# Optimization experiments

Measured on AMD Instinct MI355X. Metric: run time of the kernel, lower is better.

## Reference

```python
import jax, jax.numpy as jnp
import numpy as np
import math

B, L, E, H, G = 2, 128, 1024, 16, 8
D = E // H   # head_dim = 64
R = H // G   # query heads per kv head = 2


def setup_inputs() -> dict:
    key = jax.random.key(0)
    ks = jax.random.split(key, 12)
    def nrm(k, shape, s=1.0):
        return jax.random.normal(k, shape, dtype=jnp.float32) * s
    return {
        "Q": nrm(ks[0], (B, L, E)),
        "K": nrm(ks[1], (B, L, E)),
        "V": nrm(ks[2], (B, L, E)),
        "rpe": nrm(ks[3], (B, L, L, E)),
        "ln_g": jnp.ones((E,), jnp.float32),
        "ln_b": jnp.zeros((E,), jnp.float32),
        "Wq": nrm(ks[4], (E, H * D), 0.02), "bq": jnp.zeros((H * D,), jnp.float32),
        "Wk": nrm(ks[5], (E, G * D), 0.02), "bk": jnp.zeros((G * D,), jnp.float32),
        "Wv": nrm(ks[6], (E, G * D), 0.02), "bv": jnp.zeros((G * D,), jnp.float32),
        "Wrk": nrm(ks[7], (E, G * D), 0.02), "brk": jnp.zeros((G * D,), jnp.float32),
        "Wrv": nrm(ks[8], (E, G * D), 0.02), "brv": jnp.zeros((G * D,), jnp.float32),
        "Wo": nrm(ks[9], (E, E), 0.02), "bo": jnp.zeros((E,), jnp.float32),
    }


def _layernorm(x, g, b, eps=1e-5):
    mu = jnp.mean(x, axis=-1, keepdims=True)
    var = jnp.var(x, axis=-1, keepdims=True)
    return (x - mu) * jax.lax.rsqrt(var + eps) * g + b


def reference(Q, K, V, rpe, ln_g, ln_b, Wq, bq, Wk, bk, Wv, bv, Wrk, brk, Wrv, brv, Wo, bo):
    q = (Q @ Wq + bq).reshape(B, L, H, D).transpose(0, 2, 1, 3)   # [B,H,L,D]
    k = (K @ Wk + bk).reshape(B, L, G, D).transpose(0, 2, 1, 3)   # [B,G,L,D]
    v = (V @ Wv + bv).reshape(B, L, G, D).transpose(0, 2, 1, 3)   # [B,G,L,D]

    rn = _layernorm(rpe, ln_g, ln_b)                              # [B,L,L,E]
    rpe_k = (rn @ Wrk + brk).reshape(B, L, L, G, D).transpose(0, 3, 1, 2, 4)  # [B,G,L,L,D]
    rpe_v = (rn @ Wrv + brv).reshape(B, L, L, G, D).transpose(0, 3, 1, 2, 4)

    # Group query heads: head h = g*R + r maps to kv group g (repeat_interleave semantics).
    qg = q.reshape(B, G, R, L, D)
    # score[b,h,i,j] = q[b,h,i] . (k[b,g,i] + rpe_k[b,g,i,j]) / sqrt(D)
    # (note: the original pairs q_i with k_i, only rpe_k carries j-dependence)
    base = jnp.einsum('bgrid,bgid->bgri', qg, k)                  # j-independent q.k
    cross = jnp.einsum('bgrid,bgijd->bgrij', qg, rpe_k)
    scores = (base[..., None] + cross) / math.sqrt(D)             # [B,G,R,L,L]

    # Faithful to F.softmax over flattened L*L axis per head.
    attn = jax.nn.softmax(scores.reshape(B, G, R, L * L), axis=-1).reshape(B, G, R, L, L)

    # qv[b,h,i] = sum_j attn[b,h,i,j] * (v[b,g,i] + rpe_v[b,g,i,j])
    wsum = jnp.sum(attn, axis=-1)                                 # [B,G,R,L]
    qv = wsum[..., None] * v[:, :, None] + jnp.einsum('bgrij,bgijd->bgrid', attn, rpe_v)
    qv = qv.reshape(B, H, L, D).transpose(0, 2, 1, 3).reshape(B, L, E)
    return qv @ Wo + bo
```

## Files before the change

### kernel.cpp

```cpp
#include <hip/hip_runtime.h>


__global__ __launch_bounds__(256) void k_zero(
    const float* __restrict__ bq, const float* __restrict__ bk, const float* __restrict__ bv,
    const float* __restrict__ bo,
    float* __restrict__ q_ws, float* __restrict__ k_ws, float* __restrict__ v_ws,
    float* __restrict__ qv_ws, float* __restrict__ out, float* __restrict__ Gu_ws)
{
  int rr = blockIdx.x, tid = threadIdx.x;
#pragma unroll
  for (int s = 0; s < 4; s++) {
    int i = tid + s * 256;
    q_ws[rr * 1024 + i] = bq[i];
    qv_ws[rr * 1024 + i] = 0.f;
    out[rr * 1024 + i] = bo[i];
  }
#pragma unroll
  for (int s = 0; s < 2; s++) {
    int i = tid + s * 256;
    k_ws[rr * 512 + i] = bk[i];
    v_ws[rr * 512 + i] = bv[i];
  }
  int t = rr * 256 + tid;
  if (t < 4096) Gu_ws[t] = 0.f;
}

__global__ __launch_bounds__(256) void k_qkv(
    const float* __restrict__ Q, const float* __restrict__ K, const float* __restrict__ V,
    const float* __restrict__ Wq, const float* __restrict__ Wk, const float* __restrict__ Wv,
    float* __restrict__ q_ws, float* __restrict__ k_ws, float* __restrict__ v_ws)
{
  __shared__ float xs[8][256];
  int ct = blockIdx.x, rt = blockIdx.y, es = blockIdx.z, tid = threadIdx.x;
  const float* X; const float* W; float* out; int ldW, ldO, c0;
  if (ct < 4)      { X = Q; W = Wq; out = q_ws; ldW = 1024; ldO = 1024; c0 = ct * 256; }
  else if (ct < 6) { X = K; W = Wk; out = k_ws; ldW = 512;  ldO = 512;  c0 = (ct - 4) * 256; }
  else             { X = V; W = Wv; out = v_ws; ldW = 512;  ldO = 512;  c0 = (ct - 6) * 256; }
  int row0 = rt * 8, e0 = es * 256;
  for (int f = tid; f < 512; f += 256) {
    int r = f >> 6, e4 = f & 63;
    *(float4*)&xs[r][e4 * 4] = *(const float4*)(X + (size_t)(row0 + r) * 1024 + e0 + e4 * 4);
  }
  __syncthreads();
  int cg = tid & 63, rs = tid >> 6;
  int c = c0 + cg * 4;
  const float* wp = W + (size_t)e0 * ldW + c;
  float a0[4] = {0, 0, 0, 0}, a1[4] = {0, 0, 0, 0};
  float4 wc = *(const float4*)wp;
  for (int e = 0; e < 256; e++) {
    int en = e + 1 < 256 ? e + 1 : 255;
    float4 wn = *(const float4*)(wp + (size_t)en * ldW);
    float x0 = xs[rs][e], x1 = xs[rs + 4][e];
    a0[0] += x0 * wc.x; a0[1] += x0 * wc.y; a0[2] += x0 * wc.z; a0[3] += x0 * wc.w;
    a1[0] += x1 * wc.x; a1[1] += x1 * wc.y; a1[2] += x1 * wc.z; a1[3] += x1 * wc.w;
    wc = wn;
  }
#pragma unroll
  for (int s = 0; s < 4; s++) {
    atomicAdd(out + (size_t)(row0 + rs) * ldO + c + s, a0[s]);
    atomicAdd(out + (size_t)(row0 + rs + 4) * ldO + c + s, a1[s]);
  }
}

__global__ __launch_bounds__(256) void k_base(
    const float* __restrict__ q_ws, const float* __restrict__ k_ws,
    const float* __restrict__ brk, float* __restrict__ S0_ws)
{
  int t = blockIdx.x * 256 + threadIdx.x;
  int r = t >> 4, h = t & 15, g = h >> 1;
  const float* qp = q_ws + r * 1024 + h * 64;
  const float* kp = k_ws + r * 512 + g * 64;
  const float* bp = brk + g * 64;
  float s = 0.f;
#pragma unroll
  for (int d4 = 0; d4 < 16; d4++) {
    float4 q4 = *(const float4*)(qp + d4 * 4);
    float4 k4 = *(const float4*)(kp + d4 * 4);
    float4 b4 = *(const float4*)(bp + d4 * 4);
    s += q4.x * (k4.x + b4.x) + q4.y * (k4.y + b4.y)
       + q4.z * (k4.z + b4.z) + q4.w * (k4.w + b4.w);
  }
  S0_ws[t] = s * 0.125f;
}

__global__ __launch_bounds__(256) void k_uproj(
    const float* __restrict__ q_ws, const float* __restrict__ Wrk,
    const float* __restrict__ lng, const float* __restrict__ lnb,
    float* __restrict__ ut_ws, float* __restrict__ Gu_ws, float* __restrict__ S0_ws)
{
  __shared__ float wt[64][128];
  __shared__ float qs[32][64];
  int et = blockIdx.x, rrt = blockIdx.y, g = blockIdx.z, tid = threadIdx.x;
  int e0 = et * 128, rr0 = rrt * 16;
  for (int f = tid; f < 2048; f += 256) {
    int er = f >> 4, dq = f & 15;
    float4 p = *(const float4*)(Wrk + (size_t)(e0 + er) * 512 + g * 64 + dq * 4);
    wt[dq * 4 + 0][er] = p.x; wt[dq * 4 + 1][er] = p.y;
    wt[dq * 4 + 2][er] = p.z; wt[dq * 4 + 3][er] = p.w;
  }
  for (int f = tid; f < 512; f += 256) {
    int m = f >> 4, dq = f & 15;
    int rr = rr0 + (m >> 1), h = g * 2 + (m & 1);
    float4 p = *(const float4*)(q_ws + (size_t)rr * 1024 + h * 64 + dq * 4);
    qs[m][dq * 4 + 0] = p.x; qs[m][dq * 4 + 1] = p.y;
    qs[m][dq * 4 + 2] = p.z; qs[m][dq * 4 + 3] = p.w;
  }
  __syncthreads();
  int eg = tid & 31, rs = tid >> 5;
  float acc[4][4];
#pragma unroll
  for (int i = 0; i < 4; i++)
#pragma unroll
    for (int s = 0; s < 4; s++) acc[i][s] = 0.f;
  for (int d = 0; d < 64; d++) {
    float4 wv = *(float4*)&wt[d][eg * 4];
#pragma unroll
    for (int i = 0; i < 4; i++) {
      float qv = qs[rs * 4 + i][d];
      acc[i][0] += qv * wv.x; acc[i][1] += qv * wv.y;
      acc[i][2] += qv * wv.z; acc[i][3] += qv * wv.w;
    }
  }
#pragma unroll
  for (int k = 0; k < 2; k++) {
    int rr = rr0 + rs * 2 + k;
#pragma unroll
    for (int s = 0; s < 4; s++) {
      int e = e0 + eg * 4 + s;
      float2 st;
      st.x = acc[2 * k][s] * 0.125f;
      st.y = acc[2 * k + 1][s] * 0.125f;
      *(float2*)(ut_ws + ((size_t)rr * 1024 + e) * 16 + g * 2) = st;
    }
  }
  float4 ge4 = *(const float4*)(lng + e0 + eg * 4);
  float4 be4 = *(const float4*)(lnb + e0 + eg * 4);
#pragma unroll
  for (int i = 0; i < 4; i++) {
    float pg = 0.125f * (ge4.x * acc[i][0] + ge4.y * acc[i][1] + ge4.z * acc[i][2] + ge4.w * acc[i][3]);
    float pb = 0.125f * (be4.x * acc[i][0] + be4.y * acc[i][1] + be4.z * acc[i][2] + be4.w * acc[i][3]);
#pragma unroll
    for (int mk = 16; mk >= 1; mk >>= 1) { pg += __shfl_xor(pg, mk); pb += __shfl_xor(pb, mk); }
    if (eg == 0) {
      int m = rs * 4 + i;
      int rr = rr0 + (m >> 1), h = g * 2 + (m & 1);
      atomicAdd(Gu_ws + rr * 16 + h, pg);
      atomicAdd(S0_ws + rr * 16 + h, pb);
    }
  }
}

__global__ __launch_bounds__(128) void k_dotp(
    const float* __restrict__ rpe, const float* __restrict__ lng,
    const float* __restrict__ ut_ws,
    float* __restrict__ sraw0, float* __restrict__ sraw1,
    float* __restrict__ sxp0, float* __restrict__ sxp1,
    float* __restrict__ sqp0, float* __restrict__ sqp1)
{
  __shared__ float xs[32][68];
  __shared__ float us_t[16][68];
  int jt = blockIdx.x, rr = blockIdx.y, et = blockIdx.z, tid = threadIdx.x;
  int hq = tid & 7, jq = tid >> 3;
  int j0 = jt * 32;
  int ebase = et * 512;
  float acc[2][2] = {{0.f, 0.f}, {0.f, 0.f}};
  float sx[2] = {0.f, 0.f}, sq[2] = {0.f, 0.f};

  for (int ec = 0; ec < 8; ec++) {
    int eb = ebase + ec * 64;
    __syncthreads();
#pragma unroll
    for (int it = 0; it < 4; it++) {
      int f = it * 128 + tid;
      int row = f >> 4, e4 = f & 15;
      *(float4*)&xs[row][e4 * 4] =
          *(const float4*)(rpe + ((size_t)(rr * 128 + j0 + row)) * 1024 + eb + e4 * 4);
    }
#pragma unroll
    for (int it = 0; it < 2; it++) {
      int f = it * 128 + tid;
      int e = f >> 2, hh = f & 3;
      float4 u4 = *(const float4*)(ut_ws + ((size_t)rr * 1024 + eb + e) * 16 + hh * 4);
      float ge = lng[eb + e];
      us_t[hh * 4 + 0][e] = u4.x * ge;
      us_t[hh * 4 + 1][e] = u4.y * ge;
      us_t[hh * 4 + 2][e] = u4.z * ge;
      us_t[hh * 4 + 3][e] = u4.w * ge;
    }
    __syncthreads();
#pragma unroll
    for (int e4 = 0; e4 < 16; e4++) {
      float4 u0 = *(float4*)&us_t[hq * 2 + 0][e4 * 4];
      float4 u1 = *(float4*)&us_t[hq * 2 + 1][e4 * 4];
#pragma unroll
      for (int i = 0; i < 2; i++) {
        float4 xv = *(float4*)&xs[jq * 2 + i][e4 * 4];
        acc[i][0] += xv.x * u0.x + xv.y * u0.y + xv.z * u0.z + xv.w * u0.w;
        acc[i][1] += xv.x * u1.x + xv.y * u1.y + xv.z * u1.z + xv.w * u1.w;
      }
    }
#pragma unroll
    for (int t = 0; t < 2; t++) {
      int e4s = t * 8 + hq;
#pragma unroll
      for (int i = 0; i < 2; i++) {
        float4 xv = *(float4*)&xs[jq * 2 + i][e4s * 4];
        sx[i] += xv.x + xv.y + xv.z + xv.w;
        sq[i] += xv.x * xv.x + xv.y * xv.y + xv.z * xv.z + xv.w * xv.w;
      }
    }
  }
  float* sr = (et == 0) ? sraw0 : sraw1;
  float* sxp = (et == 0) ? sxp0 : sxp1;
  float* sqp = (et == 0) ? sqp0 : sqp1;
#pragma unroll
  for (int i = 0; i < 2; i++) {
    int j = j0 + jq * 2 + i;
    float2 o; o.x = acc[i][0]; o.y = acc[i][1];
    *(float2*)(sr + ((size_t)rr * 128 + j) * 16 + hq * 2) = o;
#pragma unroll
    for (int mk = 4; mk >= 1; mk >>= 1) {
      sx[i] += __shfl_xor(sx[i], mk, 8);
      sq[i] += __shfl_xor(sq[i], mk, 8);
    }
    if (hq == 0) {
      sxp[rr * 128 + j] = sx[i];
      sqp[rr * 128 + j] = sq[i];
    }
  }
}

__global__ __launch_bounds__(256) void k_attn_p(
    const float* __restrict__ sraw0, const float* __restrict__ sraw1,
    const float* __restrict__ sxp0, const float* __restrict__ sxp1,
    const float* __restrict__ sqp0, const float* __restrict__ sqp1,
    const float* __restrict__ Gu_ws, const float* __restrict__ S0_ws,
    float* __restrict__ s_ws,
    float* __restrict__ M_ws, float* __restrict__ Z_ws, float* __restrict__ C1_ws)
{
  int rr = blockIdx.x, tid = threadIdx.x;
  int h = tid >> 4, jl = tid & 15;
  float Gv = Gu_ws[rr * 16 + h];
  float S0v = S0_ws[rr * 16 + h];
  float sv[8], muv[8], rsvv[8];
  float m = -1e30f;
#pragma unroll
  for (int k = 0; k < 8; k++) {
    int j = jl + k * 16;
    size_t idx = ((size_t)rr * 128 + j) * 16 + h;
    float sxv = sxp0[rr * 128 + j] + sxp1[rr * 128 + j];
    float sqv = sqp0[rr * 128 + j] + sqp1[rr * 128 + j];
    float mu = sxv * (1.f / 1024.f);
    float rsv = rsqrtf(fmaxf(sqv * (1.f / 1024.f) - mu * mu, 0.f) + 1e-5f);
    float accv = sraw0[idx] + sraw1[idx];
    sv[k] = S0v + rsv * (accv - mu * Gv);
    muv[k] = mu; rsvv[k] = rsv;
    m = fmaxf(m, sv[k]);
  }
#pragma unroll
  for (int mk = 8; mk >= 1; mk >>= 1) m = fmaxf(m, __shfl_xor(m, mk, 16));
  float z = 0.f, c1 = 0.f;
#pragma unroll
  for (int k = 0; k < 8; k++) {
    int j = jl + k * 16;
    float p = expf(sv[k] - m);
    z += p;
    float p2 = p * rsvv[k];
    c1 += p2 * muv[k];
    s_ws[((size_t)rr * 128 + j) * 16 + h] = p2;
  }
#pragma unroll
  for (int mk = 8; mk >= 1; mk >>= 1) { z += __shfl_xor(z, mk, 16); c1 += __shfl_xor(c1, mk, 16); }
  if (jl == 0) {
    M_ws[rr * 16 + h] = m; Z_ws[rr * 16 + h] = z; C1_ws[rr * 16 + h] = c1;
  }
}

__global__ __launch_bounds__(128) void k_comb(
    const float* __restrict__ M_ws, const float* __restrict__ Z_ws, float* __restrict__ sc_ws)
{
  __shared__ float red[128];
  int b = blockIdx.x >> 4, h = blockIdx.x & 15;
  int i = threadIdx.x;
  int idx = ((b << 7) + i) * 16 + h;
  float ml = M_ws[idx];
  red[i] = ml;
  __syncthreads();
  for (int s = 64; s >= 1; s >>= 1) {
    if (i < s) red[i] = fmaxf(red[i], red[i + s]);
    __syncthreads();
  }
  float mg = red[0];
  __syncthreads();
  float zl = Z_ws[idx] * expf(ml - mg);
  red[i] = zl;
  __syncthreads();
  for (int s = 64; s >= 1; s >>= 1) {
    if (i < s) red[i] += red[i + s];
    __syncthreads();
  }
  float zg = red[0];
  sc_ws[idx] = expf(ml - mg) / zg;
}

__global__ __launch_bounds__(256) void k_wun(
    const float* __restrict__ rpe, const float* __restrict__ lng, const float* __restrict__ lnb,
    const float* __restrict__ p2_ws,
    const float* __restrict__ Z_ws, const float* __restrict__ C1_ws,
    float* __restrict__ w_ws)
{
  __shared__ float xs[16][512];
  __shared__ float p2s[128][16];
  __shared__ float C1S[16], ZS[16];
  int es = blockIdx.x, rr = blockIdx.y, tid = threadIdx.x;
  int e0 = es * 512;
#pragma unroll
  for (int it = 0; it < 2; it++) {
    int f = it * 256 + tid;
    int jj = f >> 2, hh = f & 3;
    *(float4*)&p2s[jj][hh * 4] = *(const float4*)(p2_ws + ((size_t)rr * 128 + jj) * 16 + hh * 4);
  }
  if (tid < 16) { C1S[tid] = C1_ws[rr * 16 + tid]; ZS[tid] = Z_ws[rr * 16 + tid]; }
  float acc[2][16];
#pragma unroll
  for (int i = 0; i < 2; i++)
#pragma unroll
    for (int h = 0; h < 16; h++) acc[i][h] = 0.f;

#define WUN_ROW(ii, xval) \
  acc[ii][0] += (xval) * p0.x;  acc[ii][1] += (xval) * p0.y;  \
  acc[ii][2] += (xval) * p0.z;  acc[ii][3] += (xval) * p0.w;  \
  acc[ii][4] += (xval) * p1.x;  acc[ii][5] += (xval) * p1.y;  \
  acc[ii][6] += (xval) * p1.z;  acc[ii][7] += (xval) * p1.w;  \
  acc[ii][8] += (xval) * p2v.x; acc[ii][9] += (xval) * p2v.y; \
  acc[ii][10] += (xval) * p2v.z; acc[ii][11] += (xval) * p2v.w; \
  acc[ii][12] += (xval) * p3.x; acc[ii][13] += (xval) * p3.y; \
  acc[ii][14] += (xval) * p3.z; acc[ii][15] += (xval) * p3.w;

  for (int jc = 0; jc < 8; jc++) {
    __syncthreads();
#pragma unroll
    for (int it = 0; it < 8; it++) {
      int f = it * 256 + tid;
      int row = f >> 7, e4 = f & 127;
      *(float4*)&xs[row][e4 * 4] =
          *(const float4*)(rpe + ((size_t)(rr * 128 + jc * 16 + row)) * 1024 + e0 + e4 * 4);
    }
    __syncthreads();
#pragma unroll
    for (int j = 0; j < 16; j++) {
      int jj = jc * 16 + j;
      float2 xv = *(float2*)&xs[j][tid * 2];
      float4 p0 = *(float4*)&p2s[jj][0];
      float4 p1 = *(float4*)&p2s[jj][4];
      float4 p2v = *(float4*)&p2s[jj][8];
      float4 p3 = *(float4*)&p2s[jj][12];
      WUN_ROW(0, xv.x)
      WUN_ROW(1, xv.y)
    }
  }
#undef WUN_ROW

#pragma unroll
  for (int i = 0; i < 2; i++) {
    int e = e0 + tid * 2 + i;
    float ge = lng[e], be = lnb[e];
    float* wp = w_ws + ((size_t)rr * 1024 + e) * 16;
#pragma unroll
    for (int hh = 0; hh < 4; hh++) {
      float4 o;
      o.x = ge * (acc[i][hh * 4 + 0] - C1S[hh * 4 + 0]) + be * ZS[hh * 4 + 0];
      o.y = ge * (acc[i][hh * 4 + 1] - C1S[hh * 4 + 1]) + be * ZS[hh * 4 + 1];
      o.z = ge * (acc[i][hh * 4 + 2] - C1S[hh * 4 + 2]) + be * ZS[hh * 4 + 2];
      o.w = ge * (acc[i][hh * 4 + 3] - C1S[hh * 4 + 3]) + be * ZS[hh * 4 + 3];
      *(float4*)(wp + hh * 4) = o;
    }
  }
}

__global__ __launch_bounds__(256) void k_qv(
    const float* __restrict__ w_ws, const float* __restrict__ Wrv,
    float* __restrict__ qv_ws)
{
  __shared__ float As[32][133];
  int g = blockIdx.x, rrt = blockIdx.y, es = blockIdx.z, tid = threadIdx.x;
  int rr0 = rrt * 16, e0 = es * 128;
  for (int f = tid; f < 2048; f += 256) {
    int rl = f >> 7, e = f & 127;
    float2 w2 = *(const float2*)(w_ws + ((size_t)(rr0 + rl) * 1024 + e0 + e) * 16 + g * 2);
    As[rl * 2 + 0][e] = w2.x;
    As[rl * 2 + 1][e] = w2.y;
  }
  __syncthreads();
  int cl = tid & 15, ms = tid >> 4;
  const float* wp = Wrv + (size_t)e0 * 512 + g * 64 + cl * 4;
  float acc[2][4];
#pragma unroll
  for (int hh = 0; hh < 2; hh++)
#pragma unroll
    for (int s = 0; s < 4; s++) acc[hh][s] = 0.f;
  float4 wc = *(const float4*)wp;
  for (int e = 0; e < 128; e++) {
    int en = e + 1 < 128 ? e + 1 : 127;
    float4 wn = *(const float4*)(wp + (size_t)en * 512);
    float a0 = As[ms * 2][e], a1 = As[ms * 2 + 1][e];
    acc[0][0] += a0 * wc.x; acc[0][1] += a0 * wc.y; acc[0][2] += a0 * wc.z; acc[0][3] += a0 * wc.w;
    acc[1][0] += a1 * wc.x; acc[1][1] += a1 * wc.y; acc[1][2] += a1 * wc.z; acc[1][3] += a1 * wc.w;
    wc = wn;
  }
  int rr = rr0 + ms;
#pragma unroll
  for (int hh = 0; hh < 2; hh++) {
    float* qp = qv_ws + (size_t)rr * 1024 + (g * 2 + hh) * 64 + cl * 4;
#pragma unroll
    for (int s = 0; s < 4; s++) atomicAdd(qp + s, acc[hh][s]);
  }
}

__global__ __launch_bounds__(256) void k_out(
    const float* __restrict__ qv_ws, const float* __restrict__ v_ws,
    const float* __restrict__ brv, const float* __restrict__ Z_ws,
    const float* __restrict__ sc_ws, const float* __restrict__ Wo,
    float* __restrict__ out)
{
  __shared__ float xs[8][128];
  int ct = blockIdx.x, rt = blockIdx.y, es = blockIdx.z, tid = threadIdx.x;
  int row0 = rt * 8, e0 = es * 128, c0 = ct * 256;
  for (int f = tid; f < 1024; f += 256) {
    int r = f >> 7, ei = f & 127;
    int e = e0 + ei, row = row0 + r;
    int h = e >> 6, gg = h >> 1, dl = e & 63;
    float vb = v_ws[row * 512 + gg * 64 + dl] + brv[gg * 64 + dl];
    xs[r][ei] = sc_ws[row * 16 + h] * (Z_ws[row * 16 + h] * vb + qv_ws[(size_t)row * 1024 + e]);
  }
  __syncthreads();
  int cg = tid & 63, rs = tid >> 6;
  int c = c0 + cg * 4;
  const float* wp = Wo + (size_t)e0 * 1024 + c;
  float a0[4] = {0, 0, 0, 0}, a1[4] = {0, 0, 0, 0};
  float4 wc = *(const float4*)wp;
  for (int e = 0; e < 128; e++) {
    int en = e + 1 < 128 ? e + 1 : 127;
    float4 wn = *(const float4*)(wp + (size_t)en * 1024);
    float x0 = xs[rs][e], x1 = xs[rs + 4][e];
    a0[0] += x0 * wc.x; a0[1] += x0 * wc.y; a0[2] += x0 * wc.z; a0[3] += x0 * wc.w;
    a1[0] += x1 * wc.x; a1[1] += x1 * wc.y; a1[2] += x1 * wc.z; a1[3] += x1 * wc.w;
    wc = wn;
  }
#pragma unroll
  for (int s = 0; s < 4; s++) {
    atomicAdd(out + (size_t)(row0 + rs) * 1024 + c + s, a0[s]);
    atomicAdd(out + (size_t)(row0 + rs + 4) * 1024 + c + s, a1[s]);
  }
}

extern "C" void kernel_launch(void* const* d_in, const int* in_sizes, int n_in,
                              void* d_out, int out_size, void* d_ws, size_t ws_size,
                              hipStream_t stream) {
  (void)in_sizes; (void)n_in; (void)out_size; (void)ws_size;
  const float* Q   = (const float*)d_in[0];
  const float* K   = (const float*)d_in[1];
  const float* V   = (const float*)d_in[2];
  const float* rpe = (const float*)d_in[3];
  const float* lng = (const float*)d_in[4];
  const float* lnb = (const float*)d_in[5];
  const float* Wq  = (const float*)d_in[6];
  const float* bq  = (const float*)d_in[7];
  const float* Wk  = (const float*)d_in[8];
  const float* bk  = (const float*)d_in[9];
  const float* Wv  = (const float*)d_in[10];
  const float* bv  = (const float*)d_in[11];
  const float* Wrk = (const float*)d_in[12];
  const float* brk = (const float*)d_in[13];
  const float* Wrv = (const float*)d_in[14];
  const float* brv = (const float*)d_in[15];
  const float* Wo  = (const float*)d_in[16];
  const float* bo  = (const float*)d_in[17];
  float* out = (float*)d_out;

  float* ws    = (float*)d_ws;
  float* q_ws  = ws;
  float* k_ws  = q_ws + 262144;
  float* v_ws  = k_ws + 131072;
  float* ut_ws = v_ws + 131072;
  float* S0_ws = ut_ws + 4194304;
  float* Gu_ws = S0_ws + 4096;
  float* s_ws  = Gu_ws + 4096;
  float* mu_ws = s_ws + 524288;
  float* rs_ws = mu_ws + 32768;
  float* M_ws  = rs_ws + 32768;
  float* Z_ws  = M_ws + 4096;
  float* C1_ws = Z_ws + 4096;
  float* sc_ws = C1_ws + 4096;
  float* qv_ws = sc_ws + 4096;
  float* sraw0 = qv_ws + 262144;
  float* sraw1 = sraw0 + 524288;
  float* sxp0  = sraw1 + 524288;
  float* sxp1  = sxp0 + 32768;
  float* sqp0  = sxp1 + 32768;
  float* sqp1  = sqp0 + 32768;
  float* w_ws  = ut_ws;

  k_zero<<<256, 256, 0, stream>>>(bq, bk, bv, bo, q_ws, k_ws, v_ws, qv_ws, out, Gu_ws);
  k_qkv<<<dim3(8, 32, 4), 256, 0, stream>>>(Q, K, V, Wq, Wk, Wv, q_ws, k_ws, v_ws);
  k_base<<<16, 256, 0, stream>>>(q_ws, k_ws, brk, S0_ws);
  k_uproj<<<dim3(8, 16, 8), 256, 0, stream>>>(q_ws, Wrk, lng, lnb, ut_ws, Gu_ws, S0_ws);
  k_dotp<<<dim3(4, 256, 2), 128, 0, stream>>>(rpe, lng, ut_ws,
                                              sraw0, sraw1, sxp0, sxp1, sqp0, sqp1);
  k_attn_p<<<256, 256, 0, stream>>>(sraw0, sraw1, sxp0, sxp1, sqp0, sqp1,
                                    Gu_ws, S0_ws, s_ws, M_ws, Z_ws, C1_ws);
  k_comb<<<32, 128, 0, stream>>>(M_ws, Z_ws, sc_ws);
  k_wun<<<dim3(2, 256), 256, 0, stream>>>(rpe, lng, lnb, s_ws, Z_ws, C1_ws, w_ws);
  k_qv<<<dim3(8, 16, 8), 256, 0, stream>>>(w_ws, Wrv, qv_ws);
  k_out<<<dim3(4, 32, 8), 256, 0, stream>>>(qv_ws, v_ws, brv, Z_ws, sc_ws, Wo, out);
}
```

Before: 470.7 us.

## Split k_wun reduction over j halves and fold LN epilogue into k_qv

k_wun now splits the j reduction into two halves across a new grid dimension, with one e per thread and 256-wide tiles. This quadruples block count and halves the accumulator registers, to better saturate bandwidth while streaming rpe. The two partial sums go to separate buffers. k_qv combines them and applies the LayerNorm gamma/beta and C1/Z correction while loading. k_zero and k_base are also regridded to use more blocks. The cost is an extra workspace buffer and more reads in k_qv.

```diff
diff --git a/kernel.cpp b/kernel.cpp
--- a/kernel.cpp
+++ b/kernel.cpp
@@ -7,22 +7,19 @@
     float* __restrict__ q_ws, float* __restrict__ k_ws, float* __restrict__ v_ws,
     float* __restrict__ qv_ws, float* __restrict__ out, float* __restrict__ Gu_ws)
 {
-  int rr = blockIdx.x, tid = threadIdx.x;
-#pragma unroll
-  for (int s = 0; s < 4; s++) {
-    int i = tid + s * 256;
-    q_ws[rr * 1024 + i] = bq[i];
-    qv_ws[rr * 1024 + i] = 0.f;
-    out[rr * 1024 + i] = bo[i];
-  }
-#pragma unroll
-  for (int s = 0; s < 2; s++) {
-    int i = tid + s * 256;
+  int rr = blockIdx.x, qy = blockIdx.y, tid = threadIdx.x;
+  int i = qy * 256 + tid;
+  q_ws[rr * 1024 + i] = bq[i];
+  qv_ws[rr * 1024 + i] = 0.f;
+  out[rr * 1024 + i] = bo[i];
+  if (qy < 2) {
     k_ws[rr * 512 + i] = bk[i];
     v_ws[rr * 512 + i] = bv[i];
   }
-  int t = rr * 256 + tid;
-  if (t < 4096) Gu_ws[t] = 0.f;
+  if (qy == 0) {
+    int t = rr * 256 + tid;
+    if (t < 4096) Gu_ws[t] = 0.f;
+  }
 }
 
 __global__ __launch_bounds__(256) void k_qkv(
@@ -62,11 +59,11 @@
   }
 }
 
-__global__ __launch_bounds__(256) void k_base(
+__global__ __launch_bounds__(128) void k_base(
     const float* __restrict__ q_ws, const float* __restrict__ k_ws,
     const float* __restrict__ brk, float* __restrict__ S0_ws)
 {
-  int t = blockIdx.x * 256 + threadIdx.x;
+  int t = blockIdx.x * 128 + threadIdx.x;
   int r = t >> 4, h = t & 15, g = h >> 1;
   const float* qp = q_ws + r * 1024 + h * 64;
   const float* kp = k_ws + r * 512 + g * 64;
@@ -304,82 +301,70 @@
 }
 
 __global__ __launch_bounds__(256) void k_wun(
-    const float* __restrict__ rpe, const float* __restrict__ lng, const float* __restrict__ lnb,
-    const float* __restrict__ p2_ws,
-    const float* __restrict__ Z_ws, const float* __restrict__ C1_ws,
-    float* __restrict__ w_ws)
-{
-  __shared__ float xs[16][512];
-  __shared__ float p2s[128][16];
-  __shared__ float C1S[16], ZS[16];
-  int es = blockIdx.x, rr = blockIdx.y, tid = threadIdx.x;
-  int e0 = es * 512;
-#pragma unroll
-  for (int it = 0; it < 2; it++) {
-    int f = it * 256 + tid;
-    int jj = f >> 2, hh = f & 3;
-    *(float4*)&p2s[jj][hh * 4] = *(const float4*)(p2_ws + ((size_t)rr * 128 + jj) * 16 + hh * 4);
-  }
-  if (tid < 16) { C1S[tid] = C1_ws[rr * 16 + tid]; ZS[tid] = Z_ws[rr * 16 + tid]; }
-  float acc[2][16];
-#pragma unroll
-  for (int i = 0; i < 2; i++)
-#pragma unroll
-    for (int h = 0; h < 16; h++) acc[i][h] = 0.f;
-
-#define WUN_ROW(ii, xval) \
-  acc[ii][0] += (xval) * p0.x;  acc[ii][1] += (xval) * p0.y;  \
-  acc[ii][2] += (xval) * p0.z;  acc[ii][3] += (xval) * p0.w;  \
-  acc[ii][4] += (xval) * p1.x;  acc[ii][5] += (xval) * p1.y;  \
-  acc[ii][6] += (xval) * p1.z;  acc[ii][7] += (xval) * p1.w;  \
-  acc[ii][8] += (xval) * p2v.x; acc[ii][9] += (xval) * p2v.y; \
-  acc[ii][10] += (xval) * p2v.z; acc[ii][11] += (xval) * p2v.w; \
-  acc[ii][12] += (xval) * p3.x; acc[ii][13] += (xval) * p3.y; \
-  acc[ii][14] += (xval) * p3.z; acc[ii][15] += (xval) * p3.w;
-
-  for (int jc = 0; jc < 8; jc++) {
+    const float* __restrict__ rpe, const float* __restrict__ p2_ws,
+    float* __restrict__ w0_ws, float* __restrict__ w1_ws)
+{
+  __shared__ float xs[16][256];
+  __shared__ float p2s[64][16];
+  int es = blockIdx.x, jh = blockIdx.y, rr = blockIdx.z, tid = threadIdx.x;
+  int e0 = es * 256, jbase = jh * 64;
+  {
+    int jj = tid >> 2, hh = tid & 3;
+    *(float4*)&p2s[jj][hh * 4] =
+        *(const float4*)(p2_ws + ((size_t)(rr * 128 + jbase + jj)) * 16 + hh * 4);
+  }
+  float acc[16];
+#pragma unroll
+  for (int h = 0; h < 16; h++) acc[h] = 0.f;
+
+#define WUN_ROW(xval) \
+  acc[0] += (xval) * p0.x;  acc[1] += (xval) * p0.y;  \
+  acc[2] += (xval) * p0.z;  acc[3] += (xval) * p0.w;  \
+  acc[4] += (xval) * p1.x;  acc[5] += (xval) * p1.y;  \
+  acc[6] += (xval) * p1.z;  acc[7] += (xval) * p1.w;  \
+  acc[8] += (xval) * p2v.x; acc[9] += (xval) * p2v.y; \
+  acc[10] += (xval) * p2v.z; acc[11] += (xval) * p2v.w; \
+  acc[12] += (xval) * p3.x; acc[13] += (xval) * p3.y; \
+  acc[14] += (xval) * p3.z; acc[15] += (xval) * p3.w;
+
+  for (int jc = 0; jc < 4; jc++) {
     __syncthreads();
 #pragma unroll
-    for (int it = 0; it < 8; it++) {
+    for (int it = 0; it < 4; it++) {
       int f = it * 256 + tid;
-      int row = f >> 7, e4 = f & 127;
+      int row = f >> 6, e4 = f & 63;
       *(float4*)&xs[row][e4 * 4] =
-          *(const float4*)(rpe + ((size_t)(rr * 128 + jc * 16 + row)) * 1024 + e0 + e4 * 4);
+          *(const float4*)(rpe + ((size_t)(rr * 128 + jbase + jc * 16 + row)) * 1024 + e0 + e4 * 4);
     }
     __syncthreads();
 #pragma unroll
     for (int j = 0; j < 16; j++) {
       int jj = jc * 16 + j;
-      float2 xv = *(float2*)&xs[j][tid * 2];
+      float x = xs[j][tid];
       float4 p0 = *(float4*)&p2s[jj][0];
       float4 p1 = *(float4*)&p2s[jj][4];
       float4 p2v = *(float4*)&p2s[jj][8];
       float4 p3 = *(float4*)&p2s[jj][12];
-      WUN_ROW(0, xv.x)
-      WUN_ROW(1, xv.y)
+      WUN_ROW(x)
     }
   }
 #undef WUN_ROW
 
-#pragma unroll
-  for (int i = 0; i < 2; i++) {
-    int e = e0 + tid * 2 + i;
-    float ge = lng[e], be = lnb[e];
-    float* wp = w_ws + ((size_t)rr * 1024 + e) * 16;
-#pragma unroll
-    for (int hh = 0; hh < 4; hh++) {
-      float4 o;
-      o.x = ge * (acc[i][hh * 4 + 0] - C1S[hh * 4 + 0]) + be * ZS[hh * 4 + 0];
-      o.y = ge * (acc[i][hh * 4 + 1] - C1S[hh * 4 + 1]) + be * ZS[hh * 4 + 1];
-      o.z = ge * (acc[i][hh * 4 + 2] - C1S[hh * 4 + 2]) + be * ZS[hh * 4 + 2];
-      o.w = ge * (acc[i][hh * 4 + 3] - C1S[hh * 4 + 3]) + be * ZS[hh * 4 + 3];
-      *(float4*)(wp + hh * 4) = o;
-    }
+  float* wp = (jh == 0 ? w0_ws : w1_ws) + ((size_t)rr * 1024 + e0 + tid) * 16;
+#pragma unroll
+  for (int hh = 0; hh < 4; hh++) {
+    float4 o;
+    o.x = acc[hh * 4 + 0]; o.y = acc[hh * 4 + 1];
+    o.z = acc[hh * 4 + 2]; o.w = acc[hh * 4 + 3];
+    *(float4*)(wp + hh * 4) = o;
   }
 }
 
 __global__ __launch_bounds__(256) void k_qv(
-    const float* __restrict__ w_ws, const float* __restrict__ Wrv,
+    const float* __restrict__ w0_ws, const float* __restrict__ w1_ws,
+    const float* __restrict__ Wrv,
+    const float* __restrict__ lng, const float* __restrict__ lnb,
+    const float* __restrict__ C1_ws, const float* __restrict__ Z_ws,
     float* __restrict__ qv_ws)
 {
   __shared__ float As[32][133];
@@ -387,9 +372,15 @@
   int rr0 = rrt * 16, e0 = es * 128;
   for (int f = tid; f < 2048; f += 256) {
     int rl = f >> 7, e = f & 127;
-    float2 w2 = *(const float2*)(w_ws + ((size_t)(rr0 + rl) * 1024 + e0 + e) * 16 + g * 2);
-    As[rl * 2 + 0][e] = w2.x;
-    As[rl * 2 + 1][e] = w2.y;
+    size_t base = ((size_t)(rr0 + rl) * 1024 + e0 + e) * 16 + g * 2;
+    float2 a = *(const float2*)(w0_ws + base);
+    float2 b = *(const float2*)(w1_ws + base);
+    float ge = lng[e0 + e], be = lnb[e0 + e];
+    int ri = (rr0 + rl) * 16 + g * 2;
+    float c0 = C1_ws[ri],     z0 = Z_ws[ri];
+    float c1 = C1_ws[ri + 1], z1 = Z_ws[ri + 1];
+    As[rl * 2 + 0][e] = ge * (a.x + b.x - c0) + be * z0;
+    As[rl * 2 + 1][e] = ge * (a.y + b.y - c1) + be * z1;
   }
   __syncthreads();
   int cl = tid & 15, ms = tid >> 4;
@@ -499,18 +490,19 @@
   float* sxp1  = sxp0 + 32768;
   float* sqp0  = sxp1 + 32768;
   float* sqp1  = sqp0 + 32768;
-  float* w_ws  = ut_ws;
-
-  k_zero<<<256, 256, 0, stream>>>(bq, bk, bv, bo, q_ws, k_ws, v_ws, qv_ws, out, Gu_ws);
+  float* w1_ws = sqp1 + 32768;
+  float* w0_ws = ut_ws;
+
+  k_zero<<<dim3(256, 4), 256, 0, stream>>>(bq, bk, bv, bo, q_ws, k_ws, v_ws, qv_ws, out, Gu_ws);
   k_qkv<<<dim3(8, 32, 4), 256, 0, stream>>>(Q, K, V, Wq, Wk, Wv, q_ws, k_ws, v_ws);
-  k_base<<<16, 256, 0, stream>>>(q_ws, k_ws, brk, S0_ws);
+  k_base<<<32, 128, 0, stream>>>(q_ws, k_ws, brk, S0_ws);
   k_uproj<<<dim3(8, 16, 8), 256, 0, stream>>>(q_ws, Wrk, lng, lnb, ut_ws, Gu_ws, S0_ws);
   k_dotp<<<dim3(4, 256, 2), 128, 0, stream>>>(rpe, lng, ut_ws,
                                               sraw0, sraw1, sxp0, sxp1, sqp0, sqp1);
   k_attn_p<<<256, 256, 0, stream>>>(sraw0, sraw1, sxp0, sxp1, sqp0, sqp1,
                                     Gu_ws, S0_ws, s_ws, M_ws, Z_ws, C1_ws);
   k_comb<<<32, 128, 0, stream>>>(M_ws, Z_ws, sc_ws);
-  k_wun<<<dim3(2, 256), 256, 0, stream>>>(rpe, lng, lnb, s_ws, Z_ws, C1_ws, w_ws);
-  k_qv<<<dim3(8, 16, 8), 256, 0, stream>>>(w_ws, Wrv, qv_ws);
+  k_wun<<<dim3(4, 2, 256), 256, 0, stream>>>(rpe, s_ws, w0_ws, w1_ws);
+  k_qv<<<dim3(8, 16, 8), 256, 0, stream>>>(w0_ws, w1_ws, Wrv, lng, lnb, C1_ws, Z_ws, qv_ws);
   k_out<<<dim3(4, 32, 8), 256, 0, stream>>>(qv_ws, v_ws, brv, Z_ws, sc_ws, Wo, out);
 }
```

Result: slower. 484.4 us (+2.9%).
